# Kernel tuning notes

Hardware: AMD Instinct MI355X
Metric: run time of the kernel (lower is better)

## Reference

```python
import jax, jax.numpy as jnp
import numpy as np

MAX_DISP = 48


def setup_inputs() -> dict:
    key = jax.random.key(0)
    k1, k2 = jax.random.split(key)
    left = jax.random.normal(k1, (2, 64, 256, 32), dtype=jnp.float32)
    right = jax.random.normal(k2, (2, 64, 256, 32), dtype=jnp.float32)
    return {"left": left, "right": right}


def reference(left, right):
    # left, right: [B, H, W, C] NHWC feature maps.
    # For each disparity d in [-D, D): out[b, d+D, h, w] = concat(left[b,h,w], right[b,h,w-d])
    # where positions with (w - d) out of [0, W) are zeroed (matches TF concat+pad semantics:
    # the pad zeroes BOTH the left and right channel halves in the invalid region).
    B, H, W, C = left.shape
    disps = jnp.arange(-MAX_DISP, MAX_DISP)          # [2D]
    w_idx = jnp.arange(W)                            # [W]

    def level(d):
        idx = w_idx - d                              # right-image column for each output column
        valid = (idx >= 0) & (idx < W)               # [W]
        r = jnp.take(right, jnp.clip(idx, 0, W - 1), axis=2)   # [B,H,W,C]
        lvl = jnp.concatenate([left, r], axis=-1)               # [B,H,W,2C]
        return jnp.where(valid[None, None, :, None], lvl, jnp.zeros((), lvl.dtype))

    cv = jax.vmap(level)(disps)                      # [2D, B, H, W, 2C]
    return jnp.transpose(cv, (1, 0, 2, 3, 4))        # [B, 2D, H, W, 2C]
```

## Files before the change

kernel.cpp:

```cpp
#include <hip/hip_runtime.h>


#define BB 2
#define D2 96
#define HH 64
#define WW 256
#define CC 32

#define TOTAL4 50331648

__global__ __launch_bounds__(256) void cost_concat_kernel(
    const float4* __restrict__ left4,
    const float4* __restrict__ right4,
    float4* __restrict__ out4)
{
    const int stride = gridDim.x * blockDim.x;
    for (int i = blockIdx.x * blockDim.x + threadIdx.x; i < TOTAL4; i += stride) {
        const int c4 = i & 15;
        int t = i >> 4;
        const int w = t & 255;  t >>= 8;
        const int h = t & 63;   t >>= 6;
        const int dd = t % D2;
        const int b  = t / D2;
        const int d  = dd - 48;
        const int idx = w - d;
        const bool valid = (idx >= 0) & (idx < WW);

        float4 v = make_float4(0.f, 0.f, 0.f, 0.f);
        if (valid) {
            if (c4 < 8) {
                v = left4[((b * HH + h) * WW + w) * 8 + c4];
            } else {
                v = right4[((b * HH + h) * WW + idx) * 8 + (c4 - 8)];
            }
        }
        out4[i] = v;
    }
}

extern "C" void kernel_launch(void* const* d_in, const int* in_sizes, int n_in,
                              void* d_out, int out_size, void* d_ws, size_t ws_size,
                              hipStream_t stream) {
    const float4* left4  = (const float4*)d_in[0];
    const float4* right4 = (const float4*)d_in[1];
    float4* out4 = (float4*)d_out;

    const int block = 256;
    const int grid = 2048;
    cost_concat_kernel<<<grid, block, 0, stream>>>(left4, right4, out4);
}
```

Before: 172.5 us.

## Loop over disparities per thread with nontemporal stores and split valid ranges

Each thread now owns one (b,h,w,half,channel-quad) element and iterates over all 96 disparities. It loads the left feature once and reuses it across disparities, and it splits the disparity loop into zero/valid/zero ranges so there is no per-element branch. It also replaces the grid-stride loop and its div/mod index math with bit-shifts, and writes output with nontemporal stores to avoid polluting cache. The trade-off is fewer threads, each issuing long strided store sequences.

```diff
diff --git a/kernel.cpp b/kernel.cpp
--- a/kernel.cpp
+++ b/kernel.cpp
@@ -1,51 +1,58 @@
 #include <hip/hip_runtime.h>
 
 
-#define BB 2
-#define D2 96
-#define HH 64
-#define WW 256
-#define CC 32
+typedef float f4 __attribute__((ext_vector_type(4)));
 
-#define TOTAL4 50331648
+#define DD_STRIDE 262144
 
 __global__ __launch_bounds__(256) void cost_concat_kernel(
-    const float4* __restrict__ left4,
-    const float4* __restrict__ right4,
-    float4* __restrict__ out4)
+    const f4* __restrict__ left4,
+    const f4* __restrict__ right4,
+    f4* __restrict__ out4)
 {
-    const int stride = gridDim.x * blockDim.x;
-    for (int i = blockIdx.x * blockDim.x + threadIdx.x; i < TOTAL4; i += stride) {
-        const int c4 = i & 15;
-        int t = i >> 4;
-        const int w = t & 255;  t >>= 8;
-        const int h = t & 63;   t >>= 6;
-        const int dd = t % D2;
-        const int b  = t / D2;
-        const int d  = dd - 48;
-        const int idx = w - d;
-        const bool valid = (idx >= 0) & (idx < WW);
+    const int tid = blockIdx.x * 256 + threadIdx.x;
+    const int c3 = tid & 7;
+    const int w  = (tid >> 3) & 255;
+    const int s  = (tid >> 11) & 1;
+    const int hb = tid >> 12;
+    const int b  = hb >> 6;
+    const int h  = hb & 63;
 
-        float4 v = make_float4(0.f, 0.f, 0.f, 0.f);
-        if (valid) {
-            if (c4 < 8) {
-                v = left4[((b * HH + h) * WW + w) * 8 + c4];
-            } else {
-                v = right4[((b * HH + h) * WW + idx) * 8 + (c4 - 8)];
-            }
-        }
-        out4[i] = v;
+    const int rowBase = hb * 2048;
+
+    f4* optr = out4 + (size_t)b * 25165824 + (size_t)h * 4096
+                    + (size_t)(w * 16 + s * 8 + c3);
+
+    const int dd_lo = max(0, w - 207);
+    const int dd_hi = min(95, w + 48);
+    const f4 z = (f4){0.f, 0.f, 0.f, 0.f};
+
+    int dd = 0;
+    for (; dd < dd_lo; ++dd)
+        __builtin_nontemporal_store(z, optr + (size_t)dd * DD_STRIDE);
+
+    if (s == 0) {
+        const f4 v = left4[rowBase + w * 8 + c3];
+        #pragma unroll 4
+        for (; dd <= dd_hi; ++dd)
+            __builtin_nontemporal_store(v, optr + (size_t)dd * DD_STRIDE);
+    } else {
+        const f4* rp = right4 + rowBase + (w + 48) * 8 + c3;
+        #pragma unroll 4
+        for (; dd <= dd_hi; ++dd)
+            __builtin_nontemporal_store(rp[-(ptrdiff_t)dd * 8], optr + (size_t)dd * DD_STRIDE);
     }
+
+    for (; dd < 96; ++dd)
+        __builtin_nontemporal_store(z, optr + (size_t)dd * DD_STRIDE);
 }
 
 extern "C" void kernel_launch(void* const* d_in, const int* in_sizes, int n_in,
                               void* d_out, int out_size, void* d_ws, size_t ws_size,
                               hipStream_t stream) {
-    const float4* left4  = (const float4*)d_in[0];
-    const float4* right4 = (const float4*)d_in[1];
-    float4* out4 = (float4*)d_out;
+    const f4* left4  = (const f4*)d_in[0];
+    const f4* right4 = (const f4*)d_in[1];
+    f4* out4 = (f4*)d_out;
 
-    const int block = 256;
-    const int grid = 2048;
-    cost_concat_kernel<<<grid, block, 0, stream>>>(left4, right4, out4);
+    cost_concat_kernel<<<2048, 256, 0, stream>>>(left4, right4, out4);
 }
```

Measured after the change: 178.0 us. +3.2%, slower.
